# Kernel tuning notes

Measured on AMD Instinct MI355X. Metric: run time of the kernel, lower is better.

## Reference

```python
import jax, jax.numpy as jnp
import numpy as np

N = 50000      # nodes
C = 64         # in_channels
O = 64         # out_channels (== in_channels, required by zeros_like in original)
S = 8          # size: number of weight matrices
E = 1700000    # edges (neighbor pairs incl. self-loops), avg degree ~34


def setup_inputs() -> dict:
    key = jax.random.key(0)
    ks = jax.random.split(key, 9)
    node_tensor = jax.random.normal(ks[0], (N, C), dtype=jnp.float32)
    src = jax.random.randint(ks[1], (E,), 0, N)                 # neighbor node j
    dst = jnp.sort(jax.random.randint(ks[2], (E,), 0, N))       # center node i
    sc = 1.0 / np.sqrt(C)
    W = jax.random.normal(ks[3], (S, C, O), dtype=jnp.float32) * sc   # linears weights
    b = jax.random.normal(ks[4], (S, O), dtype=jnp.float32) * sc      # linears biases
    Ws = jax.random.normal(ks[5], (C, S), dtype=jnp.float32) * sc     # source proj
    bs = jax.random.normal(ks[6], (S,), dtype=jnp.float32) * sc
    Wt = jax.random.normal(ks[7], (C, S), dtype=jnp.float32) * sc     # target proj
    bt = jax.random.normal(ks[8], (S,), dtype=jnp.float32) * sc
    return dict(node_tensor=node_tensor, src=src, dst=dst,
                W=W, b=b, Ws=Ws, bs=bs, Wt=Wt, bt=bt)


def reference(node_tensor, src, dst, W, b, Ws, bs, Wt, bt):
    # Per-node soft-assignment logits (FeaStNet)
    s = node_tensor @ Ws + bs          # [N, S] : source_tensor
    t = node_tensor @ Wt + bt          # [N, S] : target_tensor
    # Per-edge assignment: softmax over the `size` dim of source[center] + target[neighbor]
    q = jax.nn.softmax(s[dst] + t[src], axis=-1)      # [E, S]
    # Per-matrix projected node features: weighted[m] = x @ W_m + b_m
    Wx = jnp.einsum('nc,sco->sno', node_tensor, W) + b[:, None, :]   # [S, N, O]
    # msg[e] = sum_m q[e,m] * Wx[m, src[e]]; loop over small fixed S to avoid [S,E,O] blowup
    msg = q[:, 0:1] * Wx[0][src]                      # [E, O]
    for m in range(1, S):
        msg = msg + q[:, m:m + 1] * Wx[m][src]
    # Scatter-sum over each center's neighborhood, mean over the S weight matrices
    out = jax.ops.segment_sum(msg, dst, num_segments=N) / S          # [N, O]
    return out
```

## Files before the change

kernel.cpp:

```cpp
#include <hip/hip_runtime.h>
#include <hip/hip_bf16.h>


#define CDIM 64
#define SDIM 8

typedef __bf16 bf16x8 __attribute__((ext_vector_type(8)));
typedef float f32x4 __attribute__((ext_vector_type(4)));

__global__ __launch_bounds__(256) void k1_pre(
    const float* __restrict__ x, const float* __restrict__ Ws,
    const float* __restrict__ bs, const float* __restrict__ Wt,
    const float* __restrict__ bt, const float* __restrict__ W,
    const int* __restrict__ dst, float* __restrict__ ST,
    __hip_bfloat16* __restrict__ xbf, __hip_bfloat16* __restrict__ WtB,
    int* __restrict__ rowptr, int N, int E, int nb1) {
  int bid = blockIdx.x;
  if (bid >= nb1 + 128) {
    int e = (bid - nb1 - 128) * 256 + threadIdx.x;
    if (e >= E) return;
    int a = dst[e];
    int bnd = (e + 1 < E) ? dst[e + 1] : N;
    if (e == 0) {
      for (int d = 0; d <= a; ++d) rowptr[d] = 0;
    }
    for (int d = a + 1; d <= bnd; ++d) rowptr[d] = e + 1;
    return;
  }
  if (bid >= nb1) {
    int t = (bid - nb1) * 256 + threadIdx.x;
    int o = t >> 9, k = t & 511;
    WtB[t] = __float2bfloat16(W[(size_t)k * 64 + o]);
    return;
  }
  int tid = bid * 256 + threadIdx.x;
  int i = tid >> 4, m = tid & 15;
  if (i >= N) return;
  int mm = m & 7;
  const float* Wp = (m < 8) ? Ws : Wt;
  float acc = (m < 8) ? bs[mm] : bt[mm];
  const float* xr = x + (size_t)i * CDIM;
#pragma unroll
  for (int c = 0; c < CDIM; ++c) acc += xr[c] * Wp[c * SDIM + mm];
  ST[i * 16 + m] = acc;
  float4 xv4 = *(const float4*)(xr + m * 4);
  union { __hip_bfloat16 h[4]; ushort4 u; } cv;
  cv.h[0] = __float2bfloat16(xv4.x);
  cv.h[1] = __float2bfloat16(xv4.y);
  cv.h[2] = __float2bfloat16(xv4.z);
  cv.h[3] = __float2bfloat16(xv4.w);
  *(ushort4*)(xbf + (size_t)i * CDIM + m * 4) = cv.u;
}

__global__ __launch_bounds__(256) void k3_fused(
    const __hip_bfloat16* __restrict__ xbf, const int* __restrict__ src,
    const int* __restrict__ rowptr, const float* __restrict__ ST,
    __hip_bfloat16* __restrict__ Gbf, float* __restrict__ R, int N) {
  __shared__ float qlds[4][64];
  int wave = __builtin_amdgcn_readfirstlane(threadIdx.x >> 6);
  int lane = threadIdx.x & 63;
  int i = blockIdx.x * 4 + wave;
  if (i >= N) return;

  int lo = rowptr[i];
  int hi = rowptr[i + 1];
  int mm = lane & 7;
  int kk = lane >> 3;

  float sv = ST[i * 16 + mm];

  float g[8] = {0, 0, 0, 0, 0, 0, 0, 0};
  float racc = 0.f;
  float* qw = &qlds[wave][0];

  if (lo < hi) {
    int ecl = hi - 1;
    int ek = lo + kk;
    int iv = src[ek < ecl ? ek : ecl];

    for (int e0 = lo; e0 < hi; e0 += 8) {
      int e0n = e0 + 8;
      int ekn = e0n + kk;
      int ivn = (e0n < hi) ? src[ekn < ecl ? ekn : ecl] : iv;

      int j0 = __builtin_amdgcn_readlane(iv, 0);
      int j1 = __builtin_amdgcn_readlane(iv, 8);
      int j2 = __builtin_amdgcn_readlane(iv, 16);
      int j3 = __builtin_amdgcn_readlane(iv, 24);
      int j4 = __builtin_amdgcn_readlane(iv, 32);
      int j5 = __builtin_amdgcn_readlane(iv, 40);
      int j6 = __builtin_amdgcn_readlane(iv, 48);
      int j7 = __builtin_amdgcn_readlane(iv, 56);

      float tv = ST[iv * 16 + 8 + mm];

      float xv[8];
      xv[0] = __bfloat162float(xbf[(size_t)j0 * CDIM + lane]);
      xv[1] = __bfloat162float(xbf[(size_t)j1 * CDIM + lane]);
      xv[2] = __bfloat162float(xbf[(size_t)j2 * CDIM + lane]);
      xv[3] = __bfloat162float(xbf[(size_t)j3 * CDIM + lane]);
      xv[4] = __bfloat162float(xbf[(size_t)j4 * CDIM + lane]);
      xv[5] = __bfloat162float(xbf[(size_t)j5 * CDIM + lane]);
      xv[6] = __bfloat162float(xbf[(size_t)j6 * CDIM + lane]);
      xv[7] = __bfloat162float(xbf[(size_t)j7 * CDIM + lane]);

      float z = sv + tv;
      float mx = fmaxf(z, __shfl_xor(z, 1));
      mx = fmaxf(mx, __shfl_xor(mx, 2));
      mx = fmaxf(mx, __shfl_xor(mx, 4));
      float ez = __expf(z - mx);
      float ssum = ez + __shfl_xor(ez, 1);
      ssum += __shfl_xor(ssum, 2);
      ssum += __shfl_xor(ssum, 4);
      float qv = ez * __frcp_rn(ssum);
      if (e0 + kk >= hi) qv = 0.f;
      racc += qv;
      qw[lane] = qv;

#pragma unroll
      for (int k = 0; k < 8; ++k) {
        float4 qa = *(const float4*)(qw + k * 8);
        float4 qb = *(const float4*)(qw + k * 8 + 4);
        float xk = xv[k];
        g[0] = fmaf(qa.x, xk, g[0]);
        g[1] = fmaf(qa.y, xk, g[1]);
        g[2] = fmaf(qa.z, xk, g[2]);
        g[3] = fmaf(qa.w, xk, g[3]);
        g[4] = fmaf(qb.x, xk, g[4]);
        g[5] = fmaf(qb.y, xk, g[5]);
        g[6] = fmaf(qb.z, xk, g[6]);
        g[7] = fmaf(qb.w, xk, g[7]);
      }
      iv = ivn;
    }
  }

  __hip_bfloat16* Gi = Gbf + (size_t)i * 512;
#pragma unroll
  for (int m = 0; m < 8; ++m) Gi[m * 64 + lane] = __float2bfloat16(g[m]);

  racc += __shfl_xor(racc, 8);
  racc += __shfl_xor(racc, 16);
  racc += __shfl_xor(racc, 32);
  if (lane < 8) R[(size_t)i * 8 + lane] = racc;
}

__global__ __launch_bounds__(256) void k4_mfma(
    const __hip_bfloat16* __restrict__ Gbf, const float* __restrict__ R,
    const __hip_bfloat16* __restrict__ WtB, const float* __restrict__ bias,
    float* __restrict__ out, int N) {
  __shared__ float4 btile[64 * 65];
  {
    const float4* srcp = (const float4*)WtB;
    int t = threadIdx.x;
#pragma unroll
    for (int j = 0; j < 16; ++j) {
      int ci = t + j * 256;
      btile[(ci >> 6) * 65 + (ci & 63)] = srcp[ci];
    }
  }
  __syncthreads();

  int wave = threadIdx.x >> 6;
  int lane = threadIdx.x & 63;
  int r0 = (blockIdx.x * 4 + wave) * 16;
  if (r0 >= N) return;

  int m = lane & 15;
  int q = lane >> 4;
  const __bf16* abase = (const __bf16*)(Gbf + (size_t)(r0 + m) * 512) + q * 8;
  const __bf16* lbase = (const __bf16*)btile + (size_t)m * 520 + q * 8;

  f32x4 acc0 = {0, 0, 0, 0}, acc1 = {0, 0, 0, 0};
  f32x4 acc2 = {0, 0, 0, 0}, acc3 = {0, 0, 0, 0};
#pragma unroll
  for (int kt = 0; kt < 16; ++kt) {
    bf16x8 a = *(const bf16x8*)(abase + kt * 32);
    bf16x8 b0 = *(const bf16x8*)(lbase + 0 * 520 + kt * 32);
    bf16x8 b1 = *(const bf16x8*)(lbase + 16 * 520 + kt * 32);
    bf16x8 b2 = *(const bf16x8*)(lbase + 32 * 520 + kt * 32);
    bf16x8 b3 = *(const bf16x8*)(lbase + 48 * 520 + kt * 32);
    acc0 = __builtin_amdgcn_mfma_f32_16x16x32_bf16(a, b0, acc0, 0, 0, 0);
    acc1 = __builtin_amdgcn_mfma_f32_16x16x32_bf16(a, b1, acc1, 0, 0, 0);
    acc2 = __builtin_amdgcn_mfma_f32_16x16x32_bf16(a, b2, acc2, 0, 0, 0);
    acc3 = __builtin_amdgcn_mfma_f32_16x16x32_bf16(a, b3, acc3, 0, 0, 0);
  }

#pragma unroll
  for (int v = 0; v < 4; ++v) {
    int ri = r0 + q * 4 + v;
    if (ri >= N) continue;
    const float* Ri = R + (size_t)ri * 8;
    float b0s = 0, b1s = 0, b2s = 0, b3s = 0;
#pragma unroll
    for (int mm = 0; mm < 8; ++mm) {
      float rv = Ri[mm];
      b0s = fmaf(rv, bias[mm * 64 + 0 + m], b0s);
      b1s = fmaf(rv, bias[mm * 64 + 16 + m], b1s);
      b2s = fmaf(rv, bias[mm * 64 + 32 + m], b2s);
      b3s = fmaf(rv, bias[mm * 64 + 48 + m], b3s);
    }
    float* orow = out + (size_t)ri * 64;
    orow[0 + m]  = (acc0[v] + b0s) * 0.125f;
    orow[16 + m] = (acc1[v] + b1s) * 0.125f;
    orow[32 + m] = (acc2[v] + b2s) * 0.125f;
    orow[48 + m] = (acc3[v] + b3s) * 0.125f;
  }
}

extern "C" void kernel_launch(void* const* d_in, const int* in_sizes, int n_in,
                              void* d_out, int out_size, void* d_ws, size_t ws_size,
                              hipStream_t stream) {
  const float* x  = (const float*)d_in[0];
  const int* src  = (const int*)d_in[1];
  const int* dst  = (const int*)d_in[2];
  const float* W  = (const float*)d_in[3];
  const float* b  = (const float*)d_in[4];
  const float* Ws = (const float*)d_in[5];
  const float* bs = (const float*)d_in[6];
  const float* Wt = (const float*)d_in[7];
  const float* bt = (const float*)d_in[8];
  int N = in_sizes[0] / CDIM;
  int E = in_sizes[1];
  float* out = (float*)d_out;

  float* ST = (float*)d_ws;
  __hip_bfloat16* Gbf = (__hip_bfloat16*)(ST + (size_t)N * 16);
  float* R  = (float*)(Gbf + (size_t)N * 512);
  __hip_bfloat16* WtB = (__hip_bfloat16*)(R + (size_t)N * 8);
  __hip_bfloat16* xbf = WtB + 64 * 512;
  int* rowptr = (int*)(xbf + (size_t)N * CDIM);

  int nb1 = (N * 16 + 255) / 256;
  int nbE = (E + 255) / 256;
  k1_pre<<<nb1 + 128 + nbE, 256, 0, stream>>>(x, Ws, bs, Wt, bt, W, dst, ST,
                                              xbf, WtB, rowptr, N, E, nb1);
  k3_fused<<<(N + 3) / 4, 256, 0, stream>>>(xbf, src, rowptr, ST, Gbf, R, N);
  int mtiles = (N + 15) / 16;
  k4_mfma<<<(mtiles + 3) / 4, 256, 0, stream>>>(Gbf, R, WtB, b, out, N);
}
```

Before: 176.6 us.

## Factor softmax exp into per-node terms, use readlane broadcast, drop LDS weight tile

Precomputes exp(t) per node and exp(s) per center, so the per-edge softmax is a product plus a sum reduction, with no max-subtraction or per-edge exp. The q broadcast goes through readlane instead of an LDS round trip, and the MFMA kernel reads the bf16 weights straight from global/L2 rather than staging them in shared memory. The exp factorisation drops the max-stabilisation, so large logits could overflow. Readlane with constant lanes adds scalar instructions.

Result: slower. 213.3 us (+20.8%).

```diff
diff --git a/kernel.cpp b/kernel.cpp
--- a/kernel.cpp
+++ b/kernel.cpp
@@ -7,6 +7,10 @@
 
 typedef __bf16 bf16x8 __attribute__((ext_vector_type(8)));
 typedef float f32x4 __attribute__((ext_vector_type(4)));
+
+__device__ __forceinline__ float rdlane(float v, int l) {
+  return __int_as_float(__builtin_amdgcn_readlane(__float_as_int(v), l));
+}
 
 __global__ __launch_bounds__(256) void k1_pre(
     const float* __restrict__ x, const float* __restrict__ Ws,
@@ -42,7 +46,7 @@
   const float* xr = x + (size_t)i * CDIM;
 #pragma unroll
   for (int c = 0; c < CDIM; ++c) acc += xr[c] * Wp[c * SDIM + mm];
-  ST[i * 16 + m] = acc;
+  ST[i * 16 + m] = (m < 8) ? acc : __expf(acc);
   float4 xv4 = *(const float4*)(xr + m * 4);
   union { __hip_bfloat16 h[4]; ushort4 u; } cv;
   cv.h[0] = __float2bfloat16(xv4.x);
@@ -56,7 +60,6 @@
     const __hip_bfloat16* __restrict__ xbf, const int* __restrict__ src,
     const int* __restrict__ rowptr, const float* __restrict__ ST,
     __hip_bfloat16* __restrict__ Gbf, float* __restrict__ R, int N) {
-  __shared__ float qlds[4][64];
   int wave = __builtin_amdgcn_readfirstlane(threadIdx.x >> 6);
   int lane = threadIdx.x & 63;
   int i = blockIdx.x * 4 + wave;
@@ -67,11 +70,10 @@
   int mm = lane & 7;
   int kk = lane >> 3;
 
-  float sv = ST[i * 16 + mm];
+  float uv = __expf(ST[i * 16 + mm]);
 
   float g[8] = {0, 0, 0, 0, 0, 0, 0, 0};
   float racc = 0.f;
-  float* qw = &qlds[wave][0];
 
   if (lo < hi) {
     int ecl = hi - 1;
@@ -104,32 +106,25 @@
       xv[6] = __bfloat162float(xbf[(size_t)j6 * CDIM + lane]);
       xv[7] = __bfloat162float(xbf[(size_t)j7 * CDIM + lane]);
 
-      float z = sv + tv;
-      float mx = fmaxf(z, __shfl_xor(z, 1));
-      mx = fmaxf(mx, __shfl_xor(mx, 2));
-      mx = fmaxf(mx, __shfl_xor(mx, 4));
-      float ez = __expf(z - mx);
-      float ssum = ez + __shfl_xor(ez, 1);
+      float w = uv * tv;
+      float ssum = w + __shfl_xor(w, 1);
       ssum += __shfl_xor(ssum, 2);
       ssum += __shfl_xor(ssum, 4);
-      float qv = ez * __frcp_rn(ssum);
+      float qv = w * __frcp_rn(ssum);
       if (e0 + kk >= hi) qv = 0.f;
       racc += qv;
-      qw[lane] = qv;
 
 #pragma unroll
       for (int k = 0; k < 8; ++k) {
-        float4 qa = *(const float4*)(qw + k * 8);
-        float4 qb = *(const float4*)(qw + k * 8 + 4);
         float xk = xv[k];
-        g[0] = fmaf(qa.x, xk, g[0]);
-        g[1] = fmaf(qa.y, xk, g[1]);
-        g[2] = fmaf(qa.z, xk, g[2]);
-        g[3] = fmaf(qa.w, xk, g[3]);
-        g[4] = fmaf(qb.x, xk, g[4]);
-        g[5] = fmaf(qb.y, xk, g[5]);
-        g[6] = fmaf(qb.z, xk, g[6]);
-        g[7] = fmaf(qb.w, xk, g[7]);
+        g[0] = fmaf(rdlane(qv, k * 8 + 0), xk, g[0]);
+        g[1] = fmaf(rdlane(qv, k * 8 + 1), xk, g[1]);
+        g[2] = fmaf(rdlane(qv, k * 8 + 2), xk, g[2]);
+        g[3] = fmaf(rdlane(qv, k * 8 + 3), xk, g[3]);
+        g[4] = fmaf(rdlane(qv, k * 8 + 4), xk, g[4]);
+        g[5] = fmaf(rdlane(qv, k * 8 + 5), xk, g[5]);
+        g[6] = fmaf(rdlane(qv, k * 8 + 6), xk, g[6]);
+        g[7] = fmaf(rdlane(qv, k * 8 + 7), xk, g[7]);
       }
       iv = ivn;
     }
@@ -149,18 +144,6 @@
     const __hip_bfloat16* __restrict__ Gbf, const float* __restrict__ R,
     const __hip_bfloat16* __restrict__ WtB, const float* __restrict__ bias,
     float* __restrict__ out, int N) {
-  __shared__ float4 btile[64 * 65];
-  {
-    const float4* srcp = (const float4*)WtB;
-    int t = threadIdx.x;
-#pragma unroll
-    for (int j = 0; j < 16; ++j) {
-      int ci = t + j * 256;
-      btile[(ci >> 6) * 65 + (ci & 63)] = srcp[ci];
-    }
-  }
-  __syncthreads();
-
   int wave = threadIdx.x >> 6;
   int lane = threadIdx.x & 63;
   int r0 = (blockIdx.x * 4 + wave) * 16;
@@ -169,17 +152,17 @@
   int m = lane & 15;
   int q = lane >> 4;
   const __bf16* abase = (const __bf16*)(Gbf + (size_t)(r0 + m) * 512) + q * 8;
-  const __bf16* lbase = (const __bf16*)btile + (size_t)m * 520 + q * 8;
+  const __bf16* wbase = (const __bf16*)WtB + (size_t)m * 512 + q * 8;
 
   f32x4 acc0 = {0, 0, 0, 0}, acc1 = {0, 0, 0, 0};
   f32x4 acc2 = {0, 0, 0, 0}, acc3 = {0, 0, 0, 0};
 #pragma unroll
   for (int kt = 0; kt < 16; ++kt) {
     bf16x8 a = *(const bf16x8*)(abase + kt * 32);
-    bf16x8 b0 = *(const bf16x8*)(lbase + 0 * 520 + kt * 32);
-    bf16x8 b1 = *(const bf16x8*)(lbase + 16 * 520 + kt * 32);
-    bf16x8 b2 = *(const bf16x8*)(lbase + 32 * 520 + kt * 32);
-    bf16x8 b3 = *(const bf16x8*)(lbase + 48 * 520 + kt * 32);
+    bf16x8 b0 = *(const bf16x8*)(wbase + 0 * 16 * 512 + kt * 32);
+    bf16x8 b1 = *(const bf16x8*)(wbase + 1 * 16 * 512 + kt * 32);
+    bf16x8 b2 = *(const bf16x8*)(wbase + 2 * 16 * 512 + kt * 32);
+    bf16x8 b3 = *(const bf16x8*)(wbase + 3 * 16 * 512 + kt * 32);
     acc0 = __builtin_amdgcn_mfma_f32_16x16x32_bf16(a, b0, acc0, 0, 0, 0);
     acc1 = __builtin_amdgcn_mfma_f32_16x16x32_bf16(a, b1, acc1, 0, 0, 0);
     acc2 = __builtin_amdgcn_mfma_f32_16x16x32_bf16(a, b2, acc2, 0, 0, 0);
```

## Fuse edge aggregation with MFMA projection and precompute exp of target logits

Applied to the files above, without the earlier changes.

Merges the edge-aggregation kernel and the MFMA projection kernel into one. Each block aggregates 16 nodes into LDS and then runs the 16x64x512 MFMA directly, so the bf16 G matrix and the R array no longer round-trip through global memory. Separately, the target logits are stored as exp() in the preprocessing kernel, so the per-edge softmax becomes a multiply and normalize with no max reduction and no per-edge exp. Dropping the max subtraction risks overflow for large logits. Each wave now handles four nodes in sequence, which may reduce latency hiding, and the weights are read from global memory instead of an LDS tile.

New measurement: 209.5 us. 18.6% more time.

```diff
diff --git a/kernel.cpp b/kernel.cpp
--- a/kernel.cpp
+++ b/kernel.cpp
@@ -42,7 +42,7 @@
   const float* xr = x + (size_t)i * CDIM;
 #pragma unroll
   for (int c = 0; c < CDIM; ++c) acc += xr[c] * Wp[c * SDIM + mm];
-  ST[i * 16 + m] = acc;
+  ST[i * 16 + m] = (m < 8) ? acc : __expf(acc);
   float4 xv4 = *(const float4*)(xr + m * 4);
   union { __hip_bfloat16 h[4]; ushort4 u; } cv;
   cv.h[0] = __float2bfloat16(xv4.x);
@@ -52,159 +52,124 @@
   *(ushort4*)(xbf + (size_t)i * CDIM + m * 4) = cv.u;
 }
 
-__global__ __launch_bounds__(256) void k3_fused(
+__global__ __launch_bounds__(256) void k3_full(
     const __hip_bfloat16* __restrict__ xbf, const int* __restrict__ src,
     const int* __restrict__ rowptr, const float* __restrict__ ST,
-    __hip_bfloat16* __restrict__ Gbf, float* __restrict__ R, int N) {
+    const __hip_bfloat16* __restrict__ WtB, const float* __restrict__ bias,
+    float* __restrict__ out, int N) {
+  __shared__ __hip_bfloat16 gt[16][520];
+  __shared__ float rl[16][8];
   __shared__ float qlds[4][64];
-  int wave = __builtin_amdgcn_readfirstlane(threadIdx.x >> 6);
+
+  int wave = threadIdx.x >> 6;
   int lane = threadIdx.x & 63;
-  int i = blockIdx.x * 4 + wave;
-  if (i >= N) return;
-
-  int lo = rowptr[i];
-  int hi = rowptr[i + 1];
   int mm = lane & 7;
   int kk = lane >> 3;
-
-  float sv = ST[i * 16 + mm];
-
-  float g[8] = {0, 0, 0, 0, 0, 0, 0, 0};
-  float racc = 0.f;
+  int base = blockIdx.x * 16;
   float* qw = &qlds[wave][0];
 
-  if (lo < hi) {
-    int ecl = hi - 1;
-    int ek = lo + kk;
-    int iv = src[ek < ecl ? ek : ecl];
-
-    for (int e0 = lo; e0 < hi; e0 += 8) {
-      int e0n = e0 + 8;
-      int ekn = e0n + kk;
-      int ivn = (e0n < hi) ? src[ekn < ecl ? ekn : ecl] : iv;
-
-      int j0 = __builtin_amdgcn_readlane(iv, 0);
-      int j1 = __builtin_amdgcn_readlane(iv, 8);
-      int j2 = __builtin_amdgcn_readlane(iv, 16);
-      int j3 = __builtin_amdgcn_readlane(iv, 24);
-      int j4 = __builtin_amdgcn_readlane(iv, 32);
-      int j5 = __builtin_amdgcn_readlane(iv, 40);
-      int j6 = __builtin_amdgcn_readlane(iv, 48);
-      int j7 = __builtin_amdgcn_readlane(iv, 56);
-
-      float tv = ST[iv * 16 + 8 + mm];
-
-      float xv[8];
-      xv[0] = __bfloat162float(xbf[(size_t)j0 * CDIM + lane]);
-      xv[1] = __bfloat162float(xbf[(size_t)j1 * CDIM + lane]);
-      xv[2] = __bfloat162float(xbf[(size_t)j2 * CDIM + lane]);
-      xv[3] = __bfloat162float(xbf[(size_t)j3 * CDIM + lane]);
-      xv[4] = __bfloat162float(xbf[(size_t)j4 * CDIM + lane]);
-      xv[5] = __bfloat162float(xbf[(size_t)j5 * CDIM + lane]);
-      xv[6] = __bfloat162float(xbf[(size_t)j6 * CDIM + lane]);
-      xv[7] = __bfloat162float(xbf[(size_t)j7 * CDIM + lane]);
-
-      float z = sv + tv;
-      float mx = fmaxf(z, __shfl_xor(z, 1));
-      mx = fmaxf(mx, __shfl_xor(mx, 2));
-      mx = fmaxf(mx, __shfl_xor(mx, 4));
-      float ez = __expf(z - mx);
-      float ssum = ez + __shfl_xor(ez, 1);
-      ssum += __shfl_xor(ssum, 2);
-      ssum += __shfl_xor(ssum, 4);
-      float qv = ez * __frcp_rn(ssum);
-      if (e0 + kk >= hi) qv = 0.f;
-      racc += qv;
-      qw[lane] = qv;
-
-#pragma unroll
-      for (int k = 0; k < 8; ++k) {
-        float4 qa = *(const float4*)(qw + k * 8);
-        float4 qb = *(const float4*)(qw + k * 8 + 4);
-        float xk = xv[k];
-        g[0] = fmaf(qa.x, xk, g[0]);
-        g[1] = fmaf(qa.y, xk, g[1]);
-        g[2] = fmaf(qa.z, xk, g[2]);
-        g[3] = fmaf(qa.w, xk, g[3]);
-        g[4] = fmaf(qb.x, xk, g[4]);
-        g[5] = fmaf(qb.y, xk, g[5]);
-        g[6] = fmaf(qb.z, xk, g[6]);
-        g[7] = fmaf(qb.w, xk, g[7]);
+  for (int t = 0; t < 4; ++t) {
+    int i = base + wave * 4 + t;
+    float g[8] = {0, 0, 0, 0, 0, 0, 0, 0};
+    float racc = 0.f;
+    if (i < N) {
+      int lo = rowptr[i];
+      int hi = rowptr[i + 1];
+      float uv = __expf(ST[i * 16 + mm]);
+
+      if (lo < hi) {
+        int ecl = hi - 1;
+        int ek = lo + kk;
+        int iv = src[ek < ecl ? ek : ecl];
+
+        for (int e0 = lo; e0 < hi; e0 += 8) {
+          int e0n = e0 + 8;
+          int ekn = e0n + kk;
+          int ivn = (e0n < hi) ? src[ekn < ecl ? ekn : ecl] : iv;
+
+          int j0 = __builtin_amdgcn_readlane(iv, 0);
+          int j1 = __builtin_amdgcn_readlane(iv, 8);
+          int j2 = __builtin_amdgcn_readlane(iv, 16);
+          int j3 = __builtin_amdgcn_readlane(iv, 24);
+          int j4 = __builtin_amdgcn_readlane(iv, 32);
+          int j5 = __builtin_amdgcn_readlane(iv, 40);
+          int j6 = __builtin_amdgcn_readlane(iv, 48);
+          int j7 = __builtin_amdgcn_readlane(iv, 56);
+
+          float tv = ST[iv * 16 + 8 + mm];
+
+          float xv[8];
+          xv[0] = __bfloat162float(xbf[(size_t)j0 * CDIM + lane]);
+          xv[1] = __bfloat162float(xbf[(size_t)j1 * CDIM + lane]);
+          xv[2] = __bfloat162float(xbf[(size_t)j2 * CDIM + lane]);
+          xv[3] = __bfloat162float(xbf[(size_t)j3 * CDIM + lane]);
+          xv[4] = __bfloat162float(xbf[(size_t)j4 * CDIM + lane]);
+          xv[5] = __bfloat162float(xbf[(size_t)j5 * CDIM + lane]);
+          xv[6] = __bfloat162float(xbf[(size_t)j6 * CDIM + lane]);
+          xv[7] = __bfloat162float(xbf[(size_t)j7 * CDIM + lane]);
+
+          float w = uv * tv;
+          float ssum = w + __shfl_xor(w, 1);
+          ssum += __shfl_xor(ssum, 2);
+          ssum += __shfl_xor(ssum, 4);
+          float qv = w * __frcp_rn(ssum);
+          if (e0 + kk >= hi) qv = 0.f;
+          racc += qv;
+          qw[lane] = qv;
+
+#pragma unroll
+          for (int k = 0; k < 8; ++k) {
+            float4 qa = *(const float4*)(qw + k * 8);
+            float4 qb = *(const float4*)(qw + k * 8 + 4);
+            float xk = xv[k];
+            g[0] = fmaf(qa.x, xk, g[0]);
+            g[1] = fmaf(qa.y, xk, g[1]);
+            g[2] = fmaf(qa.z, xk, g[2]);
+            g[3] = fmaf(qa.w, xk, g[3]);
+            g[4] = fmaf(qb.x, xk, g[4]);
+            g[5] = fmaf(qb.y, xk, g[5]);
+            g[6] = fmaf(qb.z, xk, g[6]);
+            g[7] = fmaf(qb.w, xk, g[7]);
+          }
+          iv = ivn;
+        }
       }
-      iv = ivn;
     }
-  }
-
-  __hip_bfloat16* Gi = Gbf + (size_t)i * 512;
-#pragma unroll
-  for (int m = 0; m < 8; ++m) Gi[m * 64 + lane] = __float2bfloat16(g[m]);
-
-  racc += __shfl_xor(racc, 8);
-  racc += __shfl_xor(racc, 16);
-  racc += __shfl_xor(racc, 32);
-  if (lane < 8) R[(size_t)i * 8 + lane] = racc;
-}
-
-__global__ __launch_bounds__(256) void k4_mfma(
-    const __hip_bfloat16* __restrict__ Gbf, const float* __restrict__ R,
-    const __hip_bfloat16* __restrict__ WtB, const float* __restrict__ bias,
-    float* __restrict__ out, int N) {
-  __shared__ float4 btile[64 * 65];
-  {
-    const float4* srcp = (const float4*)WtB;
-    int t = threadIdx.x;
-#pragma unroll
-    for (int j = 0; j < 16; ++j) {
-      int ci = t + j * 256;
-      btile[(ci >> 6) * 65 + (ci & 63)] = srcp[ci];
-    }
-  }
+    int nl = wave * 4 + t;
+#pragma unroll
+    for (int m = 0; m < 8; ++m) gt[nl][m * 64 + lane] = __float2bfloat16(g[m]);
+    racc += __shfl_xor(racc, 8);
+    racc += __shfl_xor(racc, 16);
+    racc += __shfl_xor(racc, 32);
+    if (lane < 8) rl[nl][lane] = racc;
+  }
+
   __syncthreads();
 
-  int wave = threadIdx.x >> 6;
-  int lane = threadIdx.x & 63;
-  int r0 = (blockIdx.x * 4 + wave) * 16;
-  if (r0 >= N) return;
-
-  int m = lane & 15;
+  int row = lane & 15;
   int q = lane >> 4;
-  const __bf16* abase = (const __bf16*)(Gbf + (size_t)(r0 + m) * 512) + q * 8;
-  const __bf16* lbase = (const __bf16*)btile + (size_t)m * 520 + q * 8;
-
-  f32x4 acc0 = {0, 0, 0, 0}, acc1 = {0, 0, 0, 0};
-  f32x4 acc2 = {0, 0, 0, 0}, acc3 = {0, 0, 0, 0};
+  int c0 = wave * 16;
+  const __bf16* ab = (const __bf16*)&gt[row][0] + q * 8;
+  const __bf16* wb = (const __bf16*)WtB + (size_t)(c0 + row) * 512 + q * 8;
+
+  f32x4 acc = {0, 0, 0, 0};
 #pragma unroll
   for (int kt = 0; kt < 16; ++kt) {
-    bf16x8 a = *(const bf16x8*)(abase + kt * 32);
-    bf16x8 b0 = *(const bf16x8*)(lbase + 0 * 520 + kt * 32);
-    bf16x8 b1 = *(const bf16x8*)(lbase + 16 * 520 + kt * 32);
-    bf16x8 b2 = *(const bf16x8*)(lbase + 32 * 520 + kt * 32);
-    bf16x8 b3 = *(const bf16x8*)(lbase + 48 * 520 + kt * 32);
-    acc0 = __builtin_amdgcn_mfma_f32_16x16x32_bf16(a, b0, acc0, 0, 0, 0);
-    acc1 = __builtin_amdgcn_mfma_f32_16x16x32_bf16(a, b1, acc1, 0, 0, 0);
-    acc2 = __builtin_amdgcn_mfma_f32_16x16x32_bf16(a, b2, acc2, 0, 0, 0);
-    acc3 = __builtin_amdgcn_mfma_f32_16x16x32_bf16(a, b3, acc3, 0, 0, 0);
+    bf16x8 a = *(const bf16x8*)(ab + kt * 32);
+    bf16x8 b = *(const bf16x8*)(wb + kt * 32);
+    acc = __builtin_amdgcn_mfma_f32_16x16x32_bf16(a, b, acc, 0, 0, 0);
   }
 
 #pragma unroll
   for (int v = 0; v < 4; ++v) {
-    int ri = r0 + q * 4 + v;
-    if (ri >= N) continue;
-    const float* Ri = R + (size_t)ri * 8;
-    float b0s = 0, b1s = 0, b2s = 0, b3s = 0;
-#pragma unroll
-    for (int mm = 0; mm < 8; ++mm) {
-      float rv = Ri[mm];
-      b0s = fmaf(rv, bias[mm * 64 + 0 + m], b0s);
-      b1s = fmaf(rv, bias[mm * 64 + 16 + m], b1s);
-      b2s = fmaf(rv, bias[mm * 64 + 32 + m], b2s);
-      b3s = fmaf(rv, bias[mm * 64 + 48 + m], b3s);
-    }
-    float* orow = out + (size_t)ri * 64;
-    orow[0 + m]  = (acc0[v] + b0s) * 0.125f;
-    orow[16 + m] = (acc1[v] + b1s) * 0.125f;
-    orow[32 + m] = (acc2[v] + b2s) * 0.125f;
-    orow[48 + m] = (acc3[v] + b3s) * 0.125f;
+    int nl = q * 4 + v;
+    int i = base + nl;
+    if (i >= N) continue;
+    float bsum = 0.f;
+#pragma unroll
+    for (int m = 0; m < 8; ++m)
+      bsum = fmaf(rl[nl][m], bias[m * 64 + c0 + row], bsum);
+    out[(size_t)i * 64 + c0 + row] = (acc[v] + bsum) * 0.125f;
   }
 }
 
@@ -225,9 +190,7 @@
   float* out = (float*)d_out;
 
   float* ST = (float*)d_ws;
-  __hip_bfloat16* Gbf = (__hip_bfloat16*)(ST + (size_t)N * 16);
-  float* R  = (float*)(Gbf + (size_t)N * 512);
-  __hip_bfloat16* WtB = (__hip_bfloat16*)(R + (size_t)N * 8);
+  __hip_bfloat16* WtB = (__hip_bfloat16*)(ST + (size_t)N * 16);
   __hip_bfloat16* xbf = WtB + 64 * 512;
   int* rowptr = (int*)(xbf + (size_t)N * CDIM);
 
@@ -235,7 +198,6 @@
   int nbE = (E + 255) / 256;
   k1_pre<<<nb1 + 128 + nbE, 256, 0, stream>>>(x, Ws, bs, Wt, bt, W, dst, ST,
                                               xbf, WtB, rowptr, N, E, nb1);
-  k3_fused<<<(N + 3) / 4, 256, 0, stream>>>(xbf, src, rowptr, ST, Gbf, R, N);
-  int mtiles = (N + 15) / 16;
-  k4_mfma<<<(mtiles + 3) / 4, 256, 0, stream>>>(Gbf, R, WtB, b, out, N);
+  k3_full<<<(N + 15) / 16, 256, 0, stream>>>(xbf, src, rowptr, ST, WtB, b,
+                                             out, N);
 }
```

## Use MFMA for source/target projections and factor softmax into precomputed exponentials

Applied to the files above, without the earlier changes.

The per-node source/target projection in the preprocessing kernel now runs on bf16 MFMA: each wave computes 16 nodes, replacing the scalar 64-step dot product per thread. The target logits are stored already exponentiated, and the edge kernel computes exp(s) once per node, so the per-edge softmax becomes a product and a sum with no max-reduction and no per-edge exp. This removes shuffles and transcendental work from the hot edge loop. The trade-offs are bf16 precision in the projection and a risk of overflow, since the max-subtraction that kept the softmax numerically safe is gone.

New measurement: 160.1 us. 9.4% less time.

```diff
diff --git a/kernel.cpp b/kernel.cpp
--- a/kernel.cpp
+++ b/kernel.cpp
@@ -14,10 +14,10 @@
     const float* __restrict__ bt, const float* __restrict__ W,
     const int* __restrict__ dst, float* __restrict__ ST,
     __hip_bfloat16* __restrict__ xbf, __hip_bfloat16* __restrict__ WtB,
-    int* __restrict__ rowptr, int N, int E, int nb1) {
+    int* __restrict__ rowptr, int N, int E, int nbN) {
   int bid = blockIdx.x;
-  if (bid >= nb1 + 128) {
-    int e = (bid - nb1 - 128) * 256 + threadIdx.x;
+  if (bid >= nbN + 128) {
+    int e = (bid - nbN - 128) * 256 + threadIdx.x;
     if (e >= E) return;
     int a = dst[e];
     int bnd = (e + 1 < E) ? dst[e + 1] : N;
@@ -27,29 +27,63 @@
     for (int d = a + 1; d <= bnd; ++d) rowptr[d] = e + 1;
     return;
   }
-  if (bid >= nb1) {
-    int t = (bid - nb1) * 256 + threadIdx.x;
+  if (bid >= nbN) {
+    int t = (bid - nbN) * 256 + threadIdx.x;
     int o = t >> 9, k = t & 511;
     WtB[t] = __float2bfloat16(W[(size_t)k * 64 + o]);
     return;
   }
-  int tid = bid * 256 + threadIdx.x;
-  int i = tid >> 4, m = tid & 15;
-  if (i >= N) return;
-  int mm = m & 7;
-  const float* Wp = (m < 8) ? Ws : Wt;
-  float acc = (m < 8) ? bs[mm] : bt[mm];
-  const float* xr = x + (size_t)i * CDIM;
-#pragma unroll
-  for (int c = 0; c < CDIM; ++c) acc += xr[c] * Wp[c * SDIM + mm];
-  ST[i * 16 + m] = acc;
-  float4 xv4 = *(const float4*)(xr + m * 4);
-  union { __hip_bfloat16 h[4]; ushort4 u; } cv;
-  cv.h[0] = __float2bfloat16(xv4.x);
-  cv.h[1] = __float2bfloat16(xv4.y);
-  cv.h[2] = __float2bfloat16(xv4.z);
-  cv.h[3] = __float2bfloat16(xv4.w);
-  *(ushort4*)(xbf + (size_t)i * CDIM + m * 4) = cv.u;
+
+  __shared__ __hip_bfloat16 wst[16 * 72];
+  __shared__ float bst[16];
+  int t = threadIdx.x;
+#pragma unroll
+  for (int j = 0; j < 4; ++j) {
+    int idx = t * 4 + j;
+    int n = idx >> 6, k = idx & 63;
+    float v = (n < 8) ? Ws[k * 8 + n] : Wt[k * 8 + (n - 8)];
+    wst[n * 72 + k] = __float2bfloat16(v);
+  }
+  if (t < 16) bst[t] = (t < 8) ? bs[t] : bt[t - 8];
+  __syncthreads();
+
+  int wave = t >> 6, lane = t & 63;
+  int r = lane & 15, q = lane >> 4;
+  int node = bid * 64 + wave * 16 + r;
+  int nodec = node < N ? node : N - 1;
+  const float* xr = x + (size_t)nodec * CDIM;
+
+  bf16x8 afrag[2];
+#pragma unroll
+  for (int kt = 0; kt < 2; ++kt) {
+    float4 u0 = *(const float4*)(xr + kt * 32 + q * 8);
+    float4 u1 = *(const float4*)(xr + kt * 32 + q * 8 + 4);
+    union { bf16x8 v; __hip_bfloat16 h[8]; } a;
+    a.h[0] = __float2bfloat16(u0.x); a.h[1] = __float2bfloat16(u0.y);
+    a.h[2] = __float2bfloat16(u0.z); a.h[3] = __float2bfloat16(u0.w);
+    a.h[4] = __float2bfloat16(u1.x); a.h[5] = __float2bfloat16(u1.y);
+    a.h[6] = __float2bfloat16(u1.z); a.h[7] = __float2bfloat16(u1.w);
+    afrag[kt] = a.v;
+    if (node < N)
+      *(bf16x8*)(xbf + (size_t)node * CDIM + kt * 32 + q * 8) = a.v;
+  }
+
+  bf16x8 bf0 = *(const bf16x8*)(wst + r * 72 + q * 8);
+  bf16x8 bf1 = *(const bf16x8*)(wst + r * 72 + 32 + q * 8);
+
+  f32x4 acc = {0, 0, 0, 0};
+  acc = __builtin_amdgcn_mfma_f32_16x16x32_bf16(afrag[0], bf0, acc, 0, 0, 0);
+  acc = __builtin_amdgcn_mfma_f32_16x16x32_bf16(afrag[1], bf1, acc, 0, 0, 0);
+
+  int m = lane & 15;
+#pragma unroll
+  for (int v = 0; v < 4; ++v) {
+    int nd = bid * 64 + wave * 16 + q * 4 + v;
+    if (nd >= N) continue;
+    float val = acc[v] + bst[m];
+    if (m >= 8) val = __expf(val);
+    ST[nd * 16 + m] = val;
+  }
 }
 
 __global__ __launch_bounds__(256) void k3_fused(
@@ -67,7 +101,7 @@
   int mm = lane & 7;
   int kk = lane >> 3;
 
-  float sv = ST[i * 16 + mm];
+  float uv = __expf(ST[i * 16 + mm]);
 
   float g[8] = {0, 0, 0, 0, 0, 0, 0, 0};
   float racc = 0.f;
@@ -104,15 +138,11 @@
       xv[6] = __bfloat162float(xbf[(size_t)j6 * CDIM + lane]);
       xv[7] = __bfloat162float(xbf[(size_t)j7 * CDIM + lane]);
 
-      float z = sv + tv;
-      float mx = fmaxf(z, __shfl_xor(z, 1));
-      mx = fmaxf(mx, __shfl_xor(mx, 2));
-      mx = fmaxf(mx, __shfl_xor(mx, 4));
-      float ez = __expf(z - mx);
-      float ssum = ez + __shfl_xor(ez, 1);
+      float w = uv * tv;
+      float ssum = w + __shfl_xor(w, 1);
       ssum += __shfl_xor(ssum, 2);
       ssum += __shfl_xor(ssum, 4);
-      float qv = ez * __frcp_rn(ssum);
+      float qv = w * __frcp_rn(ssum);
       if (e0 + kk >= hi) qv = 0.f;
       racc += qv;
       qw[lane] = qv;
@@ -231,10 +261,10 @@
   __hip_bfloat16* xbf = WtB + 64 * 512;
   int* rowptr = (int*)(xbf + (size_t)N * CDIM);
 
-  int nb1 = (N * 16 + 255) / 256;
+  int nbN = (N + 63) / 64;
   int nbE = (E + 255) / 256;
-  k1_pre<<<nb1 + 128 + nbE, 256, 0, stream>>>(x, Ws, bs, Wt, bt, W, dst, ST,
-                                              xbf, WtB, rowptr, N, E, nb1);
+  k1_pre<<<nbN + 128 + nbE, 256, 0, stream>>>(x, Ws, bs, Wt, bt, W, dst, ST,
+                                              xbf, WtB, rowptr, N, E, nbN);
   k3_fused<<<(N + 3) / 4, 256, 0, stream>>>(xbf, src, rowptr, ST, Gbf, R, N);
   int mtiles = (N + 15) / 16;
   k4_mfma<<<(mtiles + 3) / 4, 256, 0, stream>>>(Gbf, R, WtB, b, out, N);
```
